# Kernel optimization log

Hardware: AMD Instinct MI355X
Metric: run time of the kernel (lower is better)

Reference implementation:

```python
import jax, jax.numpy as jnp
import numpy as np

N0 = 100000
N1 = 100000
K = 16
D_MODEL = 64
D_ATTN = 32
H = 4


def setup_inputs() -> dict:
    key = jax.random.key(0)
    ks = jax.random.split(key, 12)
    inp = {
        "coords0": jax.random.normal(ks[0], (N0, 3), jnp.float32),
        "coords1": jax.random.normal(ks[1], (N1, 3), jnp.float32),
        "feats0": jax.random.normal(ks[2], (N0, D_MODEL), jnp.float32),
        "feats1": jax.random.normal(ks[3], (N1, D_MODEL), jnp.float32),
        "knn_idxs": jax.random.randint(ks[4], (1, N1, K), 0, N0, jnp.int64 if jax.config.jax_enable_x64 else jnp.int32),
        # Linear params (PyTorch Linear: y = x @ W.T + b; stored here already transposed as [in, out])
        "Wq": jax.random.normal(ks[5], (D_MODEL, D_ATTN), jnp.float32) / np.sqrt(D_MODEL),
        "bq": jnp.zeros((D_ATTN,), jnp.float32),
        "Wk": jax.random.normal(ks[6], (D_MODEL + 3, D_ATTN), jnp.float32) / np.sqrt(D_MODEL + 3),
        "bk": jnp.zeros((D_ATTN,), jnp.float32),
        "Wv": jax.random.normal(ks[7], (D_MODEL + 3, D_MODEL), jnp.float32) / np.sqrt(D_MODEL + 3),
        "bv": jnp.zeros((D_MODEL,), jnp.float32),
    }
    return inp


def reference(coords0, coords1, feats0, feats1, knn_idxs, Wq, bq, Wk, bk, Wv, bv):
    idx = knn_idxs[0]  # [N1, K] neighbor indices into cloud 0
    n1, k_ = idx.shape
    dh_attn = D_ATTN // H   # per-head query/key depth
    dh_val = D_MODEL // H   # per-head value depth

    # Irregular gathers from source cloud
    g_feats = feats0[idx]                         # [N1, K, D_MODEL]
    rel = coords0[idx] - coords1[:, None, :]      # [N1, K, 3] relative coords
    kv_in = jnp.concatenate([g_feats, rel], axis=-1)  # [N1, K, D_MODEL+3]

    # Projections + head split
    q = (feats1 @ Wq + bq).reshape(n1, H, dh_attn)                    # [N1, H, dh]
    k = (kv_in @ Wk + bk).reshape(n1, k_, H, dh_attn).transpose(0, 2, 1, 3)  # [N1, H, K, dh]
    v = (kv_in @ Wv + bv).reshape(n1, k_, H, dh_val).transpose(0, 2, 1, 3)   # [N1, H, K, dv]

    # Attention over K neighbors per point
    attn = jnp.einsum('nhd,nhkd->nhk', q, k) / np.sqrt(dh_attn).astype(np.float32)
    attn = jax.nn.softmax(attn, axis=-1)          # [N1, H, K]
    out = jnp.einsum('nhk,nhkd->nhd', attn, v)    # [N1, H, dv]
    out = out.reshape(n1, -1)                     # [N1, D_MODEL]
    return out, knn_idxs
```

## Files before the change

### kernel.cpp

```cpp
#include <hip/hip_runtime.h>


using half8   = __attribute__((ext_vector_type(8))) _Float16;
using floatx4 = __attribute__((ext_vector_type(4))) float;

template<int CTRL>
__device__ __forceinline__ float dppAdd(float x) {
    int y = __builtin_amdgcn_update_dpp(0, __float_as_int(x), CTRL, 0xF, 0xF, true);
    return x + __int_as_float(y);
}
__device__ __forceinline__ float grpSum4(float x) {
    x = dppAdd<0x124>(x);
    x = dppAdd<0x128>(x);
    return x;
}

__global__ __launch_bounds__(256) void prep_weights(
    const float* __restrict__ Wq, const float* __restrict__ Wk,
    const float* __restrict__ Wv, const float* __restrict__ coords0,
    _Float16* __restrict__ fragKV, _Float16* __restrict__ fragQ,
    floatx4* __restrict__ cpad4, int n0)
{
    const int stride = gridDim.x * 256;
    const int base = blockIdx.x * 256 + threadIdx.x;
    for (int e = base; e < 6144; e += stride) {
        int j = e & 7, ln = (e >> 3) & 63, h = (e >> 9) & 1, t = e >> 10;
        int k = h * 32 + ((ln >> 4) * 8) + j;
        int n = t * 16 + (ln & 15);
        float v = (n < 32) ? Wk[k * 32 + n] : Wv[k * 64 + (n - 32)];
        fragKV[e] = (_Float16)v;
    }
    for (int e = base; e < 2048; e += stride) {
        int j = e & 7, ln = (e >> 3) & 63, h = (e >> 9) & 1, t = e >> 10;
        int k = h * 32 + ((ln >> 4) * 8) + j;
        int n = t * 16 + (ln & 15);
        fragQ[e] = (_Float16)Wq[k * 32 + n];
    }
    for (int i = base; i < n0; i += stride) {
        floatx4 c = { coords0[(size_t)i*3+0], coords0[(size_t)i*3+1],
                      coords0[(size_t)i*3+2], 0.f };
        cpad4[i] = c;
    }
}

__global__ __launch_bounds__(256, 4) void proj_fused(
    const float* __restrict__ feats0, const float* __restrict__ feats1,
    const _Float16* __restrict__ fragKV, const _Float16* __restrict__ fragQ,
    const float* __restrict__ bq, const float* __restrict__ bk,
    const float* __restrict__ bv,
    _Float16* __restrict__ Kh, _Float16* __restrict__ Vh, float* __restrict__ Qf,
    int n0, int n1, int nbKV, int nbQ, int tiles0, int tiles1)
{
    __shared__ __align__(16) _Float16 sFrag[6144];
    __shared__ __align__(16) _Float16 sOut[6144];

    const int tid  = threadIdx.x;
    const int wave = tid >> 6;
    const int lane = tid & 63;
    const int l15  = lane & 15;
    const int quad = lane >> 4;
    const int bid  = (int)blockIdx.x;

    if (bid < nbKV) {
        half8* sF8 = (half8*)sFrag;
        const half8* fk8 = (const half8*)fragKV;
        for (int c = tid; c < 768; c += 256) sF8[c] = fk8[c];
        __syncthreads();
        const half8* bf = (const half8*)sFrag;

        float bb[6];
        #pragma unroll
        for (int t = 0; t < 6; t++) {
            int n = t * 16 + l15;
            bb[t] = (n < 32) ? bk[n] : bv[n - 32];
        }

        for (int tile = bid; tile < tiles0; tile += nbKV) {
            const int rowBase = tile * 64;
            const int m0   = rowBase + wave * 16;
            const int row  = m0 + l15;
            const int rowc = (row < n0) ? row : (n0 - 1);
            const floatx4* X4 = (const floatx4*)(feats0 + (size_t)rowc * 64);
            floatx4 f0 = X4[quad * 2 + 0], f1 = X4[quad * 2 + 1];
            floatx4 f2 = X4[quad * 2 + 8], f3 = X4[quad * 2 + 9];
            half8 a0, a1;
            a0[0]=(_Float16)f0.x; a0[1]=(_Float16)f0.y; a0[2]=(_Float16)f0.z; a0[3]=(_Float16)f0.w;
            a0[4]=(_Float16)f1.x; a0[5]=(_Float16)f1.y; a0[6]=(_Float16)f1.z; a0[7]=(_Float16)f1.w;
            a1[0]=(_Float16)f2.x; a1[1]=(_Float16)f2.y; a1[2]=(_Float16)f2.z; a1[3]=(_Float16)f2.w;
            a1[4]=(_Float16)f3.x; a1[5]=(_Float16)f3.y; a1[6]=(_Float16)f3.z; a1[7]=(_Float16)f3.w;

            floatx4 acc[6];
            #pragma unroll
            for (int t = 0; t < 6; t++) acc[t] = (floatx4){bb[t], bb[t], bb[t], bb[t]};
            #pragma unroll
            for (int t = 0; t < 6; t++) {
                acc[t] = __builtin_amdgcn_mfma_f32_16x16x32_f16(a0, bf[(t*2+0)*64 + lane], acc[t], 0,0,0);
                acc[t] = __builtin_amdgcn_mfma_f32_16x16x32_f16(a1, bf[(t*2+1)*64 + lane], acc[t], 0,0,0);
            }

            #pragma unroll
            for (int t = 0; t < 6; t++)
                #pragma unroll
                for (int r = 0; r < 4; r++)
                    sOut[(wave * 16 + quad * 4 + r) * 96 + t * 16 + l15] = (_Float16)acc[t][r];

            const half8* so8 = (const half8*)sOut;
            {
                int r = lane >> 2, ck = lane & 3;
                int gr = m0 + r;
                if (gr < n0)
                    *((half8*)(Kh + (size_t)gr * 32) + ck) = so8[(wave*16 + r) * 12 + ck];
            }
            {
                int vc = lane & 7;
                #pragma unroll
                for (int u = 0; u < 2; u++) {
                    int r = (lane >> 3) + u * 8;
                    int gr = m0 + r;
                    if (gr < n0)
                        *((half8*)(Vh + (size_t)gr * 64) + vc) = so8[(wave*16 + r) * 12 + 4 + vc];
                }
            }
        }
    } else {
        half8* sF8 = (half8*)sFrag;
        const half8* fq8 = (const half8*)fragQ;
        for (int c = tid; c < 256; c += 256) sF8[c] = fq8[c];
        __syncthreads();
        const half8* bf = (const half8*)sFrag;

        float bb[2];
        #pragma unroll
        for (int t = 0; t < 2; t++) bb[t] = bq[t * 16 + l15];

        for (int tile = bid - nbKV; tile < tiles1; tile += nbQ) {
            const int rowBase = tile * 64;
            const int m0   = rowBase + wave * 16;
            const int row  = m0 + l15;
            const int rowc = (row < n1) ? row : (n1 - 1);
            const floatx4* X4 = (const floatx4*)(feats1 + (size_t)rowc * 64);
            floatx4 f0 = X4[quad * 2 + 0], f1 = X4[quad * 2 + 1];
            floatx4 f2 = X4[quad * 2 + 8], f3 = X4[quad * 2 + 9];
            half8 a0, a1;
            a0[0]=(_Float16)f0.x; a0[1]=(_Float16)f0.y; a0[2]=(_Float16)f0.z; a0[3]=(_Float16)f0.w;
            a0[4]=(_Float16)f1.x; a0[5]=(_Float16)f1.y; a0[6]=(_Float16)f1.z; a0[7]=(_Float16)f1.w;
            a1[0]=(_Float16)f2.x; a1[1]=(_Float16)f2.y; a1[2]=(_Float16)f2.z; a1[3]=(_Float16)f2.w;
            a1[4]=(_Float16)f3.x; a1[5]=(_Float16)f3.y; a1[6]=(_Float16)f3.z; a1[7]=(_Float16)f3.w;

            floatx4 acc[2];
            #pragma unroll
            for (int t = 0; t < 2; t++) acc[t] = (floatx4){bb[t], bb[t], bb[t], bb[t]};
            #pragma unroll
            for (int t = 0; t < 2; t++) {
                acc[t] = __builtin_amdgcn_mfma_f32_16x16x32_f16(a0, bf[(t*2+0)*64 + lane], acc[t], 0,0,0);
                acc[t] = __builtin_amdgcn_mfma_f32_16x16x32_f16(a1, bf[(t*2+1)*64 + lane], acc[t], 0,0,0);
            }
            #pragma unroll
            for (int t = 0; t < 2; t++)
                #pragma unroll
                for (int r = 0; r < 4; r++) {
                    int ro = m0 + quad * 4 + r;
                    if (ro < n1) Qf[(size_t)ro * 32 + t * 16 + l15] = acc[t][r];
                }
        }
    }
}

__global__ __launch_bounds__(256, 4) void attn_kernel(
    const floatx4* __restrict__ cpad4, const float* __restrict__ coords1,
    const int*   __restrict__ knn,
    const float* __restrict__ Qf,
    const _Float16* __restrict__ Kh, const _Float16* __restrict__ Vh,
    const float* __restrict__ Wk, const float* __restrict__ Wv,
    float* __restrict__ out, float* __restrict__ outIdx, int n1)
{
    __shared__ __align__(16) float sQ[16][36];
    __shared__ float sWk3[3][32];
    __shared__ float sWv3[3][64];
    __shared__ __align__(16) float sT[16][12];
    __shared__ __align__(16) int   sIdx[16][16];
    __shared__ __align__(16) int   sIdxLin[16][16];
    __shared__ __align__(16) floatx4 sRel[16][16];
    __shared__ __align__(16) floatx4 sRbar[16][4];
    __shared__ __align__(16) float sA[16][68];

    const int tid = threadIdx.x;
    for (int e = tid; e < 288; e += 256) {
        if (e < 96) ((float*)sWk3)[e] = Wk[2048 + e];
        else        ((float*)sWv3)[e - 96] = Wv[4096 + (e - 96)];
    }
    if (tid < 128) {
        int pt = tid >> 3, c4 = tid & 7;
        int r = blockIdx.x * 16 + pt;
        if (r >= n1) r = n1 - 1;
        ((floatx4*)&sQ[pt][0])[c4] = ((const floatx4*)Qf)[(size_t)r * 8 + c4];
    }
    __syncthreads();

    const int p = tid >> 4;
    const int j = tid & 15;
    const int n = blockIdx.x * 16 + p;
    const bool valid = (n < n1);
    const int nc = valid ? n : (n1 - 1);

    const int idx = knn[nc * 16 + j];

    const int g    = j & 7;
    const int hf   = j >> 3;
    const int h    = (j >> 1) & 3;
    const int slot = ((j & 1) << 3) + (j >> 1);
    const int sub  = j >> 2;
    const int c4   = j & 3;

    sIdxLin[p][j]  = idx;
    sIdx[p][slot]  = idx;

    floatx4 cg = cpad4[idx];
    const float r0 = cg[0] - coords1[nc * 3 + 0];
    const float r1 = cg[1] - coords1[nc * 3 + 1];
    const float r2 = cg[2] - coords1[nc * 3 + 2];
    sRel[p][j] = (floatx4){r0, r1, r2, 0.f};

    if (j < 12) {
        int c = j >> 2, h2 = j & 3;
        float t = 0.f;
        #pragma unroll
        for (int i = 0; i < 8; i++)
            t = fmaf(sWk3[c][h2 * 8 + i], sQ[p][h2 * 8 + i], t);
        sT[p][j] = t;
    }

    int nbIdx[4];
    #pragma unroll
    for (int t = 0; t < 4; t++) nbIdx[t] = sIdxLin[p][t * 4 + sub];
    half8 kk[4];
    #pragma unroll
    for (int t = 0; t < 4; t++)
        kk[t] = *(const half8*)(Kh + (size_t)nbIdx[t] * 32 + c4 * 8);

    const int4* si4 = (const int4*)&sIdx[p][hf * 8];
    int4 viA = si4[0], viB = si4[1];
    int vIdx[8] = {viA.x, viA.y, viA.z, viA.w, viB.x, viB.y, viB.z, viB.w};
    half8 v8[8];
    #pragma unroll
    for (int s = 0; s < 8; s++)
        v8[s] = *(const half8*)(Vh + (size_t)vIdx[s] * 64 + g * 8);

    const float scale = 0.35355339059327373f;
    floatx4 qa = ((const floatx4*)&sQ[p][0])[c4 * 2 + 0];
    floatx4 qb = ((const floatx4*)&sQ[p][0])[c4 * 2 + 1];
    const float t0 = sT[p][0 * 4 + c4];
    const float t1 = sT[p][1 * 4 + c4];
    const float t2 = sT[p][2 * 4 + c4];

    floatx4 rl[4];
    float e[4];
    #pragma unroll
    for (int t = 0; t < 4; t++) {
        rl[t] = sRel[p][t * 4 + sub];
        float acc = rl[t][0] * t0 + rl[t][1] * t1 + rl[t][2] * t2;
        acc = fmaf(qa[0], (float)kk[t][0], acc);
        acc = fmaf(qa[1], (float)kk[t][1], acc);
        acc = fmaf(qa[2], (float)kk[t][2], acc);
        acc = fmaf(qa[3], (float)kk[t][3], acc);
        acc = fmaf(qb[0], (float)kk[t][4], acc);
        acc = fmaf(qb[1], (float)kk[t][5], acc);
        acc = fmaf(qb[2], (float)kk[t][6], acc);
        acc = fmaf(qb[3], (float)kk[t][7], acc);
        e[t] = __expf(acc * scale);
    }
    float ssum = (e[0] + e[1]) + (e[2] + e[3]);
    ssum = grpSum4(ssum);
    const float rinv = __builtin_amdgcn_rcpf(ssum);

    float a_t[4];
    #pragma unroll
    for (int t = 0; t < 4; t++) a_t[t] = e[t] * rinv;

    #pragma unroll
    for (int t = 0; t < 4; t++) {
        int nb = t * 4 + sub;
        sA[p][c4 * 16 + ((nb & 1) << 3) + (nb >> 1)] = a_t[t];
    }

    {
        float pr0 = 0.f, pr1 = 0.f, pr2 = 0.f;
        #pragma unroll
        for (int t = 0; t < 4; t++) {
            pr0 = fmaf(a_t[t], rl[t][0], pr0);
            pr1 = fmaf(a_t[t], rl[t][1], pr1);
            pr2 = fmaf(a_t[t], rl[t][2], pr2);
        }
        pr0 = grpSum4(pr0);
        pr1 = grpSum4(pr1);
        pr2 = grpSum4(pr2);
        if (sub == 0) sRbar[p][c4] = (floatx4){pr0, pr1, pr2, 0.f};
    }

    if (valid) outIdx[n * 16 + j] = (float)idx;

    const floatx4* a4 = (const floatx4*)&sA[p][h * 16 + hf * 8];
    floatx4 aw0 = a4[0], aw1 = a4[1];
    float av[8] = {aw0[0], aw0[1], aw0[2], aw0[3], aw1[0], aw1[1], aw1[2], aw1[3]};

    floatx4 rb = sRbar[p][h];

    float acc8[8] = {0,0,0,0,0,0,0,0};
    #pragma unroll
    for (int s = 0; s < 8; s++)
        #pragma unroll
        for (int i = 0; i < 8; i++)
            acc8[i] = fmaf(av[s], (float)v8[s][i], acc8[i]);

    #pragma unroll
    for (int i = 0; i < 8; i++) acc8[i] = dppAdd<0x128>(acc8[i]);

    #pragma unroll
    for (int i = 0; i < 8; i++)
        acc8[i] += rb[0] * sWv3[0][8 * g + i] + rb[1] * sWv3[1][8 * g + i] + rb[2] * sWv3[2][8 * g + i];

    if (valid) {
        floatx4 st = { acc8[hf * 4 + 0], acc8[hf * 4 + 1], acc8[hf * 4 + 2], acc8[hf * 4 + 3] };
        ((floatx4*)out)[(size_t)n * 16 + g * 2 + hf] = st;
    }
}

extern "C" void kernel_launch(void* const* d_in, const int* in_sizes, int n_in,
                              void* d_out, int out_size, void* d_ws, size_t ws_size,
                              hipStream_t stream) {
    const float* coords0 = (const float*)d_in[0];
    const float* coords1 = (const float*)d_in[1];
    const float* feats0  = (const float*)d_in[2];
    const float* feats1  = (const float*)d_in[3];
    const int*   knn     = (const int*)d_in[4];
    const float* Wq      = (const float*)d_in[5];
    const float* bq      = (const float*)d_in[6];
    const float* Wk      = (const float*)d_in[7];
    const float* bk      = (const float*)d_in[8];
    const float* Wv      = (const float*)d_in[9];
    const float* bv      = (const float*)d_in[10];

    const int n0 = in_sizes[0] / 3;
    const int n1 = in_sizes[1] / 3;

    char* ws = (char*)d_ws;
    _Float16* Kh = (_Float16*)ws;
    _Float16* Vh = (_Float16*)(ws + (size_t)n0 * 64);
    float*    Qf = (float*)(ws + (size_t)n0 * 64 + (size_t)n0 * 128);
    floatx4*  cpad4 = (floatx4*)((char*)Qf + (size_t)n1 * 128);
    _Float16* fragKV = (_Float16*)(cpad4 + n0);
    _Float16* fragQ  = fragKV + 6144;

    float* out    = (float*)d_out;
    float* outIdx = out + (size_t)n1 * 64;

    const int tiles0 = (n0 + 63) / 64;
    const int tiles1 = (n1 + 63) / 64;
    const int nbKV = 512, nbQ = 256;

    prep_weights<<<128, 256, 0, stream>>>(Wq, Wk, Wv, coords0,
                                          fragKV, fragQ, cpad4, n0);
    proj_fused<<<nbKV + nbQ, 256, 0, stream>>>(feats0, feats1, fragKV, fragQ,
                                               bq, bk, bv, Kh, Vh, Qf,
                                               n0, n1, nbKV, nbQ, tiles0, tiles1);
    attn_kernel<<<(n1 + 15) / 16, 256, 0, stream>>>(cpad4, coords1, knn,
                                                    Qf, Kh, Vh, Wk, Wv, out, outIdx, n1);
}
```

Measured before the change: 187.8 us.

## Fuse prep, projection and attention into one cooperative persistent kernel

Replaces the three launches (weight prep, projection, attention) with a single cooperative kernel of 1024 persistent blocks. Each block stages the weight fragments in shared memory, runs grid-strided projection tiles, then a grid-wide sync, then grid-strided attention groups. This removes the launch gaps between kernels and the separate weight-fragment pass through global memory. In exchange it adds a grid barrier and the per-block weight staging, and the attention phase loses the occupancy of one block per group. If the cooperative launch fails, the original three-kernel path runs.

```diff
diff --git a/kernel.cpp b/kernel.cpp
--- a/kernel.cpp
+++ b/kernel.cpp
@@ -1,4 +1,7 @@
 #include <hip/hip_runtime.h>
+#include <hip/hip_cooperative_groups.h>
+
+namespace cg = cooperative_groups;
 
 
 using half8   = __attribute__((ext_vector_type(8))) _Float16;
@@ -13,6 +16,306 @@
     x = dppAdd<0x124>(x);
     x = dppAdd<0x128>(x);
     return x;
+}
+
+__global__ __launch_bounds__(256, 4) void fused_kernel(
+    const float* __restrict__ coords0, const float* __restrict__ coords1,
+    const float* __restrict__ feats0, const float* __restrict__ feats1,
+    const int*   __restrict__ knn,
+    const float* __restrict__ Wq, const float* __restrict__ bq,
+    const float* __restrict__ Wk, const float* __restrict__ bk,
+    const float* __restrict__ Wv, const float* __restrict__ bv,
+    _Float16* __restrict__ Kh, _Float16* __restrict__ Vh,
+    float* __restrict__ Qf, floatx4* __restrict__ cpad4,
+    float* __restrict__ out, float* __restrict__ outIdx,
+    int n0, int n1, int tiles0, int tiles1, int ngroups)
+{
+    __shared__ __align__(16) char smem[28672];
+
+    const int tid  = threadIdx.x;
+    const int wave = tid >> 6;
+    const int lane = tid & 63;
+    const int l15  = lane & 15;
+    const int quad = lane >> 4;
+    const int bid  = (int)blockIdx.x;
+    const int NB   = (int)gridDim.x;
+
+    _Float16* sFragKV = (_Float16*)smem;
+    _Float16* sFragQ  = (_Float16*)(smem + 12288);
+    _Float16* sOut    = (_Float16*)(smem + 16384);
+
+    for (int e = tid; e < 6144; e += 256) {
+        int j = e & 7, ln = (e >> 3) & 63, h = (e >> 9) & 1, t = e >> 10;
+        int k = h * 32 + ((ln >> 4) * 8) + j;
+        int n = t * 16 + (ln & 15);
+        float v = (n < 32) ? Wk[k * 32 + n] : Wv[k * 64 + (n - 32)];
+        sFragKV[e] = (_Float16)v;
+    }
+    for (int e = tid; e < 2048; e += 256) {
+        int j = e & 7, ln = (e >> 3) & 63, h = (e >> 9) & 1, t = e >> 10;
+        int k = h * 32 + ((ln >> 4) * 8) + j;
+        int n = t * 16 + (ln & 15);
+        sFragQ[e] = (_Float16)Wq[k * 32 + n];
+    }
+    for (int i = bid * 256 + tid; i < n0; i += NB * 256) {
+        floatx4 c = { coords0[(size_t)i*3+0], coords0[(size_t)i*3+1],
+                      coords0[(size_t)i*3+2], 0.f };
+        cpad4[i] = c;
+    }
+    __syncthreads();
+
+    {
+        const half8* bf = (const half8*)sFragKV;
+        float bb[6];
+        #pragma unroll
+        for (int t = 0; t < 6; t++) {
+            int n = t * 16 + l15;
+            bb[t] = (n < 32) ? bk[n] : bv[n - 32];
+        }
+
+        for (int tile = bid; tile < tiles0; tile += NB) {
+            const int rowBase = tile * 64;
+            const int m0   = rowBase + wave * 16;
+            const int row  = m0 + l15;
+            const int rowc = (row < n0) ? row : (n0 - 1);
+            const floatx4* X4 = (const floatx4*)(feats0 + (size_t)rowc * 64);
+            floatx4 f0 = X4[quad * 2 + 0], f1 = X4[quad * 2 + 1];
+            floatx4 f2 = X4[quad * 2 + 8], f3 = X4[quad * 2 + 9];
+            half8 a0, a1;
+            a0[0]=(_Float16)f0.x; a0[1]=(_Float16)f0.y; a0[2]=(_Float16)f0.z; a0[3]=(_Float16)f0.w;
+            a0[4]=(_Float16)f1.x; a0[5]=(_Float16)f1.y; a0[6]=(_Float16)f1.z; a0[7]=(_Float16)f1.w;
+            a1[0]=(_Float16)f2.x; a1[1]=(_Float16)f2.y; a1[2]=(_Float16)f2.z; a1[3]=(_Float16)f2.w;
+            a1[4]=(_Float16)f3.x; a1[5]=(_Float16)f3.y; a1[6]=(_Float16)f3.z; a1[7]=(_Float16)f3.w;
+
+            floatx4 acc[6];
+            #pragma unroll
+            for (int t = 0; t < 6; t++) acc[t] = (floatx4){bb[t], bb[t], bb[t], bb[t]};
+            #pragma unroll
+            for (int t = 0; t < 6; t++) {
+                acc[t] = __builtin_amdgcn_mfma_f32_16x16x32_f16(a0, bf[(t*2+0)*64 + lane], acc[t], 0,0,0);
+                acc[t] = __builtin_amdgcn_mfma_f32_16x16x32_f16(a1, bf[(t*2+1)*64 + lane], acc[t], 0,0,0);
+            }
+
+            #pragma unroll
+            for (int t = 0; t < 6; t++)
+                #pragma unroll
+                for (int r = 0; r < 4; r++)
+                    sOut[(wave * 16 + quad * 4 + r) * 96 + t * 16 + l15] = (_Float16)acc[t][r];
+
+            const half8* so8 = (const half8*)sOut;
+            {
+                int r = lane >> 2, ck = lane & 3;
+                int gr = m0 + r;
+                if (gr < n0)
+                    *((half8*)(Kh + (size_t)gr * 32) + ck) = so8[(wave*16 + r) * 12 + ck];
+            }
+            {
+                int vc = lane & 7;
+                #pragma unroll
+                for (int u = 0; u < 2; u++) {
+                    int r = (lane >> 3) + u * 8;
+                    int gr = m0 + r;
+                    if (gr < n0)
+                        *((half8*)(Vh + (size_t)gr * 64) + vc) = so8[(wave*16 + r) * 12 + 4 + vc];
+                }
+            }
+        }
+    }
+
+    {
+        const half8* bf = (const half8*)sFragQ;
+        float bb[2];
+        #pragma unroll
+        for (int t = 0; t < 2; t++) bb[t] = bq[t * 16 + l15];
+
+        for (int tile = bid; tile < tiles1; tile += NB) {
+            const int rowBase = tile * 64;
+            const int m0   = rowBase + wave * 16;
+            const int row  = m0 + l15;
+            const int rowc = (row < n1) ? row : (n1 - 1);
+            const floatx4* X4 = (const floatx4*)(feats1 + (size_t)rowc * 64);
+            floatx4 f0 = X4[quad * 2 + 0], f1 = X4[quad * 2 + 1];
+            floatx4 f2 = X4[quad * 2 + 8], f3 = X4[quad * 2 + 9];
+            half8 a0, a1;
+            a0[0]=(_Float16)f0.x; a0[1]=(_Float16)f0.y; a0[2]=(_Float16)f0.z; a0[3]=(_Float16)f0.w;
+            a0[4]=(_Float16)f1.x; a0[5]=(_Float16)f1.y; a0[6]=(_Float16)f1.z; a0[7]=(_Float16)f1.w;
+            a1[0]=(_Float16)f2.x; a1[1]=(_Float16)f2.y; a1[2]=(_Float16)f2.z; a1[3]=(_Float16)f2.w;
+            a1[4]=(_Float16)f3.x; a1[5]=(_Float16)f3.y; a1[6]=(_Float16)f3.z; a1[7]=(_Float16)f3.w;
+
+            floatx4 acc[2];
+            #pragma unroll
+            for (int t = 0; t < 2; t++) acc[t] = (floatx4){bb[t], bb[t], bb[t], bb[t]};
+            #pragma unroll
+            for (int t = 0; t < 2; t++) {
+                acc[t] = __builtin_amdgcn_mfma_f32_16x16x32_f16(a0, bf[(t*2+0)*64 + lane], acc[t], 0,0,0);
+                acc[t] = __builtin_amdgcn_mfma_f32_16x16x32_f16(a1, bf[(t*2+1)*64 + lane], acc[t], 0,0,0);
+            }
+            #pragma unroll
+            for (int t = 0; t < 2; t++)
+                #pragma unroll
+                for (int r = 0; r < 4; r++) {
+                    int ro = m0 + quad * 4 + r;
+                    if (ro < n1) Qf[(size_t)ro * 32 + t * 16 + l15] = acc[t][r];
+                }
+        }
+    }
+
+    __threadfence();
+    cg::this_grid().sync();
+    __syncthreads();
+
+    float   (*sQ)[36]      = (float(*)[36])   (smem + 0);
+    float   (*sWk3)[32]    = (float(*)[32])   (smem + 2304);
+    float   (*sWv3)[64]    = (float(*)[64])   (smem + 2688);
+    float   (*sT)[12]      = (float(*)[12])   (smem + 3456);
+    int     (*sIdx)[16]    = (int(*)[16])     (smem + 4224);
+    int     (*sIdxLin)[16] = (int(*)[16])     (smem + 5248);
+    floatx4 (*sRel)[16]    = (floatx4(*)[16]) (smem + 6272);
+    floatx4 (*sRbar)[4]    = (floatx4(*)[4])  (smem + 10368);
+    float   (*sA)[68]      = (float(*)[68])   (smem + 11392);
+
+    for (int e = tid; e < 288; e += 256) {
+        if (e < 96) ((float*)sWk3)[e] = Wk[2048 + e];
+        else        ((float*)sWv3)[e - 96] = Wv[4096 + (e - 96)];
+    }
+
+    const int p = tid >> 4;
+    const int j = tid & 15;
+    const int g    = j & 7;
+    const int hf   = j >> 3;
+    const int h    = (j >> 1) & 3;
+    const int slot = ((j & 1) << 3) + (j >> 1);
+    const int sub  = j >> 2;
+    const int c4   = j & 3;
+
+    for (int grp = bid; grp < ngroups; grp += NB) {
+        __syncthreads();
+        if (tid < 128) {
+            int pt = tid >> 3, cq = tid & 7;
+            int r = grp * 16 + pt;
+            if (r >= n1) r = n1 - 1;
+            ((floatx4*)&sQ[pt][0])[cq] = ((const floatx4*)Qf)[(size_t)r * 8 + cq];
+        }
+        __syncthreads();
+
+        const int n = grp * 16 + p;
+        const bool valid = (n < n1);
+        const int nc = valid ? n : (n1 - 1);
+
+        const int idx = knn[nc * 16 + j];
+
+        sIdxLin[p][j]  = idx;
+        sIdx[p][slot]  = idx;
+
+        floatx4 cg4 = cpad4[idx];
+        const float r0 = cg4[0] - coords1[nc * 3 + 0];
+        const float r1 = cg4[1] - coords1[nc * 3 + 1];
+        const float r2 = cg4[2] - coords1[nc * 3 + 2];
+        sRel[p][j] = (floatx4){r0, r1, r2, 0.f};
+
+        if (j < 12) {
+            int c = j >> 2, h2 = j & 3;
+            float t = 0.f;
+            #pragma unroll
+            for (int i = 0; i < 8; i++)
+                t = fmaf(sWk3[c][h2 * 8 + i], sQ[p][h2 * 8 + i], t);
+            sT[p][j] = t;
+        }
+
+        int nbIdx[4];
+        #pragma unroll
+        for (int t = 0; t < 4; t++) nbIdx[t] = sIdxLin[p][t * 4 + sub];
+        half8 kk[4];
+        #pragma unroll
+        for (int t = 0; t < 4; t++)
+            kk[t] = *(const half8*)(Kh + (size_t)nbIdx[t] * 32 + c4 * 8);
+
+        const int4* si4 = (const int4*)&sIdx[p][hf * 8];
+        int4 viA = si4[0], viB = si4[1];
+        int vIdx[8] = {viA.x, viA.y, viA.z, viA.w, viB.x, viB.y, viB.z, viB.w};
+        half8 v8[8];
+        #pragma unroll
+        for (int s = 0; s < 8; s++)
+            v8[s] = *(const half8*)(Vh + (size_t)vIdx[s] * 64 + g * 8);
+
+        const float scale = 0.35355339059327373f;
+        floatx4 qa = ((const floatx4*)&sQ[p][0])[c4 * 2 + 0];
+        floatx4 qb = ((const floatx4*)&sQ[p][0])[c4 * 2 + 1];
+        const float t0 = sT[p][0 * 4 + c4];
+        const float t1 = sT[p][1 * 4 + c4];
+        const float t2 = sT[p][2 * 4 + c4];
+
+        floatx4 rl[4];
+        float e[4];
+        #pragma unroll
+        for (int t = 0; t < 4; t++) {
+            rl[t] = sRel[p][t * 4 + sub];
+            float acc = rl[t][0] * t0 + rl[t][1] * t1 + rl[t][2] * t2;
+            acc = fmaf(qa[0], (float)kk[t][0], acc);
+            acc = fmaf(qa[1], (float)kk[t][1], acc);
+            acc = fmaf(qa[2], (float)kk[t][2], acc);
+            acc = fmaf(qa[3], (float)kk[t][3], acc);
+            acc = fmaf(qb[0], (float)kk[t][4], acc);
+            acc = fmaf(qb[1], (float)kk[t][5], acc);
+            acc = fmaf(qb[2], (float)kk[t][6], acc);
+            acc = fmaf(qb[3], (float)kk[t][7], acc);
+            e[t] = __expf(acc * scale);
+        }
+        float ssum = (e[0] + e[1]) + (e[2] + e[3]);
+        ssum = grpSum4(ssum);
+        const float rinv = __builtin_amdgcn_rcpf(ssum);
+
+        float a_t[4];
+        #pragma unroll
+        for (int t = 0; t < 4; t++) a_t[t] = e[t] * rinv;
+
+        #pragma unroll
+        for (int t = 0; t < 4; t++) {
+            int nb = t * 4 + sub;
+            sA[p][c4 * 16 + ((nb & 1) << 3) + (nb >> 1)] = a_t[t];
+        }
+
+        {
+            float pr0 = 0.f, pr1 = 0.f, pr2 = 0.f;
+            #pragma unroll
+            for (int t = 0; t < 4; t++) {
+                pr0 = fmaf(a_t[t], rl[t][0], pr0);
+                pr1 = fmaf(a_t[t], rl[t][1], pr1);
+                pr2 = fmaf(a_t[t], rl[t][2], pr2);
+            }
+            pr0 = grpSum4(pr0);
+            pr1 = grpSum4(pr1);
+            pr2 = grpSum4(pr2);
+            if (sub == 0) sRbar[p][c4] = (floatx4){pr0, pr1, pr2, 0.f};
+        }
+
+        if (valid) outIdx[n * 16 + j] = (float)idx;
+
+        const floatx4* a4 = (const floatx4*)&sA[p][h * 16 + hf * 8];
+        floatx4 aw0 = a4[0], aw1 = a4[1];
+        float av[8] = {aw0[0], aw0[1], aw0[2], aw0[3], aw1[0], aw1[1], aw1[2], aw1[3]};
+
+        floatx4 rb = sRbar[p][h];
+
+        float acc8[8] = {0,0,0,0,0,0,0,0};
+        #pragma unroll
+        for (int s = 0; s < 8; s++)
+            #pragma unroll
+            for (int i = 0; i < 8; i++)
+                acc8[i] = fmaf(av[s], (float)v8[s][i], acc8[i]);
+
+        #pragma unroll
+        for (int i = 0; i < 8; i++) acc8[i] = dppAdd<0x128>(acc8[i]);
+
+        #pragma unroll
+        for (int i = 0; i < 8; i++)
+            acc8[i] += rb[0] * sWv3[0][8 * g + i] + rb[1] * sWv3[1][8 * g + i] + rb[2] * sWv3[2][8 * g + i];
+
+        if (valid) {
+            floatx4 st = { acc8[hf * 4 + 0], acc8[hf * 4 + 1], acc8[hf * 4 + 2], acc8[hf * 4 + 3] };
+            ((floatx4*)out)[(size_t)n * 16 + g * 2 + hf] = st;
+        }
+    }
 }
 
 __global__ __launch_bounds__(256) void prep_weights(
@@ -215,10 +518,10 @@
     sIdxLin[p][j]  = idx;
     sIdx[p][slot]  = idx;
 
-    floatx4 cg = cpad4[idx];
-    const float r0 = cg[0] - coords1[nc * 3 + 0];
-    const float r1 = cg[1] - coords1[nc * 3 + 1];
-    const float r2 = cg[2] - coords1[nc * 3 + 2];
+    floatx4 cg4 = cpad4[idx];
+    const float r0 = cg4[0] - coords1[nc * 3 + 0];
+    const float r1 = cg4[1] - coords1[nc * 3 + 1];
+    const float r2 = cg4[2] - coords1[nc * 3 + 2];
     sRel[p][j] = (floatx4){r0, r1, r2, 0.f};
 
     if (j < 12) {
@@ -356,13 +659,32 @@
 
     const int tiles0 = (n0 + 63) / 64;
     const int tiles1 = (n1 + 63) / 64;
+    const int ngroups = (n1 + 15) / 16;
+
+    {
+        _Float16* KhA = Kh; _Float16* VhA = Vh; float* QfA = Qf;
+        floatx4* cpA = cpad4; float* outA = out; float* oiA = outIdx;
+        int n0A = n0, n1A = n1, t0A = tiles0, t1A = tiles1, ngA = ngroups;
+        void* kargs[] = {
+            (void*)&coords0, (void*)&coords1, (void*)&feats0, (void*)&feats1,
+            (void*)&knn, (void*)&Wq, (void*)&bq, (void*)&Wk, (void*)&bk,
+            (void*)&Wv, (void*)&bv,
+            (void*)&KhA, (void*)&VhA, (void*)&QfA, (void*)&cpA,
+            (void*)&outA, (void*)&oiA,
+            (void*)&n0A, (void*)&n1A, (void*)&t0A, (void*)&t1A, (void*)&ngA
+        };
+        hipError_t err = hipLaunchCooperativeKernel(
+            (const void*)fused_kernel, dim3(1024), dim3(256), kargs, 0, stream);
+        if (err == hipSuccess) return;
+        (void)hipGetLastError();
+    }
+
     const int nbKV = 512, nbQ = 256;
-
     prep_weights<<<128, 256, 0, stream>>>(Wq, Wk, Wv, coords0,
                                           fragKV, fragQ, cpad4, n0);
     proj_fused<<<nbKV + nbQ, 256, 0, stream>>>(feats0, feats1, fragKV, fragQ,
                                                bq, bk, bv, Kh, Vh, Qf,
                                                n0, n1, nbKV, nbQ, tiles0, tiles1);
-    attn_kernel<<<(n1 + 15) / 16, 256, 0, stream>>>(cpad4, coords1, knn,
-                                                    Qf, Kh, Vh, Wk, Wv, out, outIdx, n1);
+    attn_kernel<<<ngroups, 256, 0, stream>>>(cpad4, coords1, knn,
+                                             Qf, Kh, Vh, Wk, Wv, out, outIdx, n1);
 }
```

New measurement: 417.0 us. +122.1%, slower.
